# Optimization experiments

Hardware: AMD Instinct MI355X
Metric: run time of the kernel (lower is better)

The kernel has to match this reference:

```python
import jax, jax.numpy as jnp
import numpy as np

B, S, D, H = 4, 2048, 1024, 16
HD = D // H  # head_dim = 64


def setup_inputs() -> dict:
    key = jax.random.key(0)
    ks = jax.random.split(key, 9)
    sc = 1.0 / np.sqrt(D)
    return {
        "x": jax.random.normal(ks[0], (B, S, D), dtype=jnp.float32),
        "Wq": jax.random.normal(ks[1], (D, D), dtype=jnp.float32) * sc,
        "bq": jnp.zeros((D,), dtype=jnp.float32),
        "Wk": jax.random.normal(ks[2], (D, D), dtype=jnp.float32) * sc,
        "bk": jnp.zeros((D,), dtype=jnp.float32),
        "Wv": jax.random.normal(ks[3], (D, D), dtype=jnp.float32) * sc,
        "bv": jnp.zeros((D,), dtype=jnp.float32),
        "Wo": jax.random.normal(ks[4], (D, D), dtype=jnp.float32) * sc,
        "bo": jnp.zeros((D,), dtype=jnp.float32),
    }


def reference(x, Wq, bq, Wk, bk, Wv, bv, Wo, bo):
    # QKV projections (torch Linear: x @ W.T + b), reshape to [B, H, S, HD]
    def proj(W, b):
        return (x @ W.T + b).reshape(B, S, H, HD).transpose(0, 2, 1, 3)

    Q, K, V = proj(Wq, bq), proj(Wk, bk), proj(Wv, bv)
    scores = jnp.einsum("bhqd,bhkd->bhqk", Q, K) / jnp.sqrt(jnp.float32(HD))
    attn = jax.nn.softmax(scores, axis=-1)  # dropout is identity at eval
    ctx = jnp.einsum("bhqk,bhkd->bhqd", attn, V)
    ctx = ctx.transpose(0, 2, 1, 3).reshape(B, S, D)
    out = ctx @ Wo.T + bo
    return out, attn
```

## Files before the change

kernel.cpp:

```cpp
#include <hip/hip_runtime.h>
#include <stdint.h>

#define Mm 8192
#define Dd 1024

typedef unsigned short u16;
typedef __attribute__((ext_vector_type(8))) short bf16x8;
typedef __attribute__((ext_vector_type(4))) float f32x4;
typedef __attribute__((ext_vector_type(4))) u16 u16x4;

__device__ __forceinline__ u16 f2bf(float f) {
  union { float f; uint32_t u; } c; c.f = f;
  uint32_t u = c.u;
  return (u16)((u + 0x7fffu + ((u >> 16) & 1u)) >> 16);
}

__device__ __forceinline__ float EXP2(float x) {
#if __has_builtin(__builtin_amdgcn_exp2f)
  return __builtin_amdgcn_exp2f(x);
#else
  return exp2f(x);
#endif
}

__device__ __forceinline__ float LOG2(float x) {
#if __has_builtin(__builtin_amdgcn_logf)
  return __builtin_amdgcn_logf(x);
#else
  return log2f(x);
#endif
}

__device__ __forceinline__ uint32_t cvtpk(float a, float b) {
  uint32_t r;
  asm("v_cvt_pk_bf16_f32 %0, %1, %2" : "=v"(r) : "v"(a), "v"(b));
  return r;
}

__device__ __forceinline__ void gll16(const void* g, void* l) {
  __builtin_amdgcn_global_load_lds((const __attribute__((address_space(1))) void*)g,
                                   (__attribute__((address_space(3))) void*)l, 16, 0, 0);
}

__global__ void cvt_all(const float* __restrict__ x, const float* __restrict__ wq,
                        const float* __restrict__ wk, const float* __restrict__ wv,
                        const float* __restrict__ wo, u16* __restrict__ out) {
  const int xn4 = 2097152, wn4 = 262144;
  const int total = xn4 + 4 * wn4;
  int i = blockIdx.x * blockDim.x + threadIdx.x;
  int stride = gridDim.x * blockDim.x;
  for (; i < total; i += stride) {
    const float* src; int off;
    if (i < xn4) { src = x; off = i; }
    else {
      int j = i - xn4; int wsel = j >> 18; off = j & (wn4 - 1);
      src = (wsel == 0) ? wq : (wsel == 1) ? wk : (wsel == 2) ? wv : wo;
    }
    float4 v = ((const float4*)src)[off];
    u16x4 o;
    o.x = f2bf(v.x); o.y = f2bf(v.y); o.z = f2bf(v.z); o.w = f2bf(v.w);
    ((u16x4*)out)[i] = o;
  }
}

template<int MODE>
__global__ __launch_bounds__(256) void gemm_bt(
    const u16* __restrict__ A, const u16* __restrict__ Bt,
    const float* __restrict__ bias, void* __restrict__ out,
    int M, int N, int K, float scale)
{
  __shared__ u16 As[128 * 32];
  __shared__ u16 Bs[128 * 32];
  int tiles_n = N >> 7;
  int nwg = (M >> 7) * tiles_n;
  int bid = blockIdx.x;
  { int q = nwg >> 3; bid = (bid & 7) * q + (bid >> 3); }
  int tm = bid / tiles_n, tn = bid % tiles_n;
  int tid = threadIdx.x;
  int wid = tid >> 6, lane = tid & 63;
  int wr = wid >> 1, wc = wid & 1;

  f32x4 acc[4][4] = {};

  int a_row = wr * 64 + (lane & 15);
  int b_row = wc * 64 + (lane & 15);
  int frag_k = (lane >> 4) * 8;

  const u16* ga0 = A + (size_t)(tm * 128 + wid * 32 + (lane >> 2)) * K + (lane & 3) * 8;
  const u16* ga1 = ga0 + (size_t)16 * K;
  const u16* gb0 = Bt + (size_t)(tn * 128 + wid * 32 + (lane >> 2)) * K + (lane & 3) * 8;
  const u16* gb1 = gb0 + (size_t)16 * K;
  u16* lA0 = As + wid * 1024;
  u16* lA1 = As + wid * 1024 + 512;
  u16* lB0 = Bs + wid * 1024;
  u16* lB1 = Bs + wid * 1024 + 512;

  for (int kt = 0; kt < K; kt += 32) {
    gll16(ga0 + kt, lA0);
    gll16(ga1 + kt, lA1);
    gll16(gb0 + kt, lB0);
    gll16(gb1 + kt, lB1);
    __syncthreads();
    bf16x8 af[4], bfr[4];
#pragma unroll
    for (int i = 0; i < 4; i++)
      af[i] = *(const bf16x8*)(As + (a_row + i * 16) * 32 + frag_k);
#pragma unroll
    for (int i = 0; i < 4; i++)
      bfr[i] = *(const bf16x8*)(Bs + (b_row + i * 16) * 32 + frag_k);
#pragma unroll
    for (int i = 0; i < 4; i++)
#pragma unroll
      for (int j = 0; j < 4; j++)
        acc[i][j] = __builtin_amdgcn_mfma_f32_16x16x32_bf16(af[i], bfr[j], acc[i][j], 0, 0, 0);
    __syncthreads();
  }

#pragma unroll
  for (int i = 0; i < 4; i++) {
#pragma unroll
    for (int j = 0; j < 4; j++) {
      int col = tn * 128 + wc * 64 + j * 16 + (lane & 15);
      float bv = bias ? bias[col] : 0.f;
#pragma unroll
      for (int r = 0; r < 4; r++) {
        int row = tm * 128 + wr * 64 + i * 16 + (lane >> 4) * 4 + r;
        float v = (acc[i][j][r] + bv) * scale;
        if (MODE == 0) {
          int b_ = row >> 11, s = row & 2047, h = col >> 6, hd = col & 63;
          ((u16*)out)[(((size_t)(b_ * 16 + h) * 2048 + s) << 6) + hd] = f2bf(v);
        } else if (MODE == 2) {
          int b_ = row >> 11, s = row & 2047, h = col >> 6, hd = col & 63;
          ((u16*)out)[((size_t)(b_ * 16 + h) * 64 + hd) * 2048 + s] = f2bf(v);
        } else {
          ((float*)out)[(size_t)row * N + col] = v;
        }
      }
    }
  }
}

__global__ __launch_bounds__(512) void attn_fused(
    const u16* __restrict__ Qb, const u16* __restrict__ Kb,
    const u16* __restrict__ Vtb, float* __restrict__ attn_out,
    u16* __restrict__ ctxb)
{
  __shared__ u16 Ks[2][4096];
  __shared__ u16 Vs[2][4096];
  __shared__ u16 Ps[8192];

  int bid = blockIdx.x;
  int swz = (bid & 7) * 128 + (bid >> 3);
  int bh = swz >> 4, qt = swz & 15;
  int tid = threadIdx.x, w = tid >> 6, lane = tid & 63;
  int g = lane >> 4, l15 = lane & 15;

  const u16* Qg = Qb + ((size_t)bh * 2048 + qt * 128) * 64;
  const u16* Kg = Kb + (size_t)bh * 2048 * 64;
  const u16* Vg = Vtb + (size_t)bh * 64 * 2048;
  float* Ag = attn_out + ((size_t)bh * 2048 + qt * 128) * 2048;

  int qloc = w * 16 + l15;
  bf16x8 aq0 = *(const bf16x8*)(Qg + (size_t)qloc * 64 + g * 8);
  bf16x8 aq1 = *(const bf16x8*)(Qg + (size_t)qloc * 64 + 32 + g * 8);

  int srow = w * 8 + (lane >> 3);
  int schunk = (lane & 7) ^ (lane >> 3);
  const u16* Ksrc = Kg + (size_t)srow * 64 + schunk * 8;
  const u16* Vsrc = Vg + (size_t)srow * 2048 + schunk * 8;

  float lsum = 0.f;
  gll16(Ksrc, (char*)Ks[0] + w * 1024);
  __syncthreads();
  for (int it = 0; it < 32; ++it) {
    int buf = it & 1;
    if (it < 31) gll16(Ksrc + (size_t)(it + 1) * 4096, (char*)Ks[buf ^ 1] + w * 1024);
    f32x4 s[4] = {};
    const char* Kbase = (const char*)Ks[buf];
#pragma unroll
    for (int t = 0; t < 4; t++) {
      int kr = t * 16 + l15;
      int x = (kr & 7) << 4;
      bf16x8 k0 = *(const bf16x8*)(Kbase + kr * 128 + ((g * 16) ^ x));
      bf16x8 k1 = *(const bf16x8*)(Kbase + kr * 128 + ((64 + g * 16) ^ x));
      s[t] = __builtin_amdgcn_mfma_f32_16x16x32_bf16(k0, aq0, s[t], 0, 0, 0);
      s[t] = __builtin_amdgcn_mfma_f32_16x16x32_bf16(k1, aq1, s[t], 0, 0, 0);
    }
#pragma unroll
    for (int t = 0; t < 4; t++)
#pragma unroll
      for (int r = 0; r < 4; r++) lsum += EXP2(s[t][r]);
    __syncthreads();
  }
  lsum += __shfl_xor(lsum, 16);
  lsum += __shfl_xor(lsum, 32);
  float lr2 = -LOG2(lsum);

  f32x4 ctx[4] = {};
  gll16(Ksrc, (char*)Ks[0] + w * 1024);
  gll16(Vsrc, (char*)Vs[0] + w * 1024);
  __syncthreads();
  int xq = (qloc & 7) << 4;
  char* Pb = (char*)Ps + qloc * 128;
  for (int it = 0; it < 32; ++it) {
    int buf = it & 1;
    if (it < 31) {
      gll16(Ksrc + (size_t)(it + 1) * 4096, (char*)Ks[buf ^ 1] + w * 1024);
      gll16(Vsrc + (size_t)(it + 1) * 64,  (char*)Vs[buf ^ 1] + w * 1024);
    }
    f32x4 s[4] = {};
    const char* Kbase = (const char*)Ks[buf];
#pragma unroll
    for (int t = 0; t < 4; t++) {
      int kr = t * 16 + l15;
      int x = (kr & 7) << 4;
      bf16x8 k0 = *(const bf16x8*)(Kbase + kr * 128 + ((g * 16) ^ x));
      bf16x8 k1 = *(const bf16x8*)(Kbase + kr * 128 + ((64 + g * 16) ^ x));
      s[t] = __builtin_amdgcn_mfma_f32_16x16x32_bf16(k0, aq0, s[t], 0, 0, 0);
      s[t] = __builtin_amdgcn_mfma_f32_16x16x32_bf16(k1, aq1, s[t], 0, 0, 0);
    }
    float* Arow = Ag + (size_t)qloc * 2048 + it * 64 + g * 4;
    uint2 pk[4];
#pragma unroll
    for (int t = 0; t < 4; t++) {
      f32x4 p;
#pragma unroll
      for (int r = 0; r < 4; r++) p[r] = EXP2(s[t][r] + lr2);
      *(f32x4*)(Arow + t * 16) = p;
      pk[t].x = cvtpk(p[0], p[1]);
      pk[t].y = cvtpk(p[2], p[3]);
    }
#pragma unroll
    for (int t = 0; t < 4; t++)
      *(uint2*)(Pb + ((t * 32 + g * 8) ^ xq)) = pk[t];
#pragma unroll
    for (int kk = 0; kk < 2; kk++) {
      bf16x8 ap = *(const bf16x8*)(Pb + ((kk * 64 + g * 16) ^ xq));
#pragma unroll
      for (int t = 0; t < 4; t++) {
        int dr = t * 16 + l15;
        bf16x8 bv = *(const bf16x8*)((const char*)Vs[buf] + dr * 128 + ((kk * 64 + g * 16) ^ ((dr & 7) << 4)));
        ctx[t] = __builtin_amdgcn_mfma_f32_16x16x32_bf16(ap, bv, ctx[t], 0, 0, 0);
      }
    }
    __syncthreads();
  }

  int b_ = bh >> 4, h = bh & 15;
#pragma unroll
  for (int t = 0; t < 4; t++)
#pragma unroll
    for (int r = 0; r < 4; r++) {
      int qg = qt * 128 + w * 16 + g * 4 + r;
      int col = h * 64 + t * 16 + l15;
      ctxb[((size_t)b_ * 2048 + qg) * 1024 + col] = f2bf(ctx[t][r]);
    }
}

extern "C" void kernel_launch(void* const* d_in, const int* in_sizes, int n_in,
                              void* d_out, int out_size, void* d_ws, size_t ws_size,
                              hipStream_t stream) {
  const float* x  = (const float*)d_in[0];
  const float* Wq = (const float*)d_in[1];
  const float* bq = (const float*)d_in[2];
  const float* Wk = (const float*)d_in[3];
  const float* bk = (const float*)d_in[4];
  const float* Wv = (const float*)d_in[5];
  const float* bv = (const float*)d_in[6];
  const float* Wo = (const float*)d_in[7];
  const float* bo = (const float*)d_in[8];

  u16* xb   = (u16*)d_ws;
  u16* Wqb  = xb + (size_t)Mm * Dd;
  u16* Wkb  = Wqb + (size_t)Dd * Dd;
  u16* Wvb  = Wkb + (size_t)Dd * Dd;
  u16* Wob  = Wvb + (size_t)Dd * Dd;
  u16* Qb   = Wob + (size_t)Dd * Dd;
  u16* Kbuf = Qb + (size_t)Mm * Dd;
  u16* Vtb  = Kbuf + (size_t)Mm * Dd;
  u16* ctxb = Vtb + (size_t)Mm * Dd;

  float* out_f = (float*)d_out;
  float* attn_o = out_f + (size_t)Mm * Dd;

  cvt_all<<<2048, 256, 0, stream>>>(x, Wq, Wk, Wv, Wo, xb);

  const float qscale = 0.125f * 1.44269504088896340736f;
  gemm_bt<0><<<512, 256, 0, stream>>>(xb, Wqb, bq, Qb,   Mm, Dd, Dd, qscale);
  gemm_bt<0><<<512, 256, 0, stream>>>(xb, Wkb, bk, Kbuf, Mm, Dd, Dd, 1.0f);
  gemm_bt<2><<<512, 256, 0, stream>>>(xb, Wvb, bv, Vtb,  Mm, Dd, Dd, 1.0f);
  attn_fused<<<1024, 512, 0, stream>>>(Qb, Kbuf, Vtb, attn_o, ctxb);
  gemm_bt<1><<<512, 256, 0, stream>>>(ctxb, Wob, bo, (void*)out_f, Mm, Dd, Dd, 1.0f);
}
```

Baseline: 519.2 us.

## Load K/V fragments directly from global memory, drop LDS staging and barriers

The attention kernel no longer stages K and V tiles through double-buffered shared memory with async loads and __syncthreads. Each wave now reads its MFMA fragments straight from global memory and relies on L1/L2 caching, with a launch-bounds occupancy hint of 4 blocks. The kernel also uses nontemporal stores for the large attention-probability output, and the V-transpose projection epilogue writes four bf16 values as one vector. The aim is to remove LDS traffic and barrier stalls and raise occupancy, at the risk of redundant global/L2 reads by all 8 waves and exposed load latency.

```diff
diff --git a/kernel.cpp b/kernel.cpp
--- a/kernel.cpp
+++ b/kernel.cpp
@@ -122,31 +122,35 @@
     for (int j = 0; j < 4; j++) {
       int col = tn * 128 + wc * 64 + j * 16 + (lane & 15);
       float bv = bias ? bias[col] : 0.f;
-#pragma unroll
-      for (int r = 0; r < 4; r++) {
-        int row = tm * 128 + wr * 64 + i * 16 + (lane >> 4) * 4 + r;
-        float v = (acc[i][j][r] + bv) * scale;
-        if (MODE == 0) {
-          int b_ = row >> 11, s = row & 2047, h = col >> 6, hd = col & 63;
-          ((u16*)out)[(((size_t)(b_ * 16 + h) * 2048 + s) << 6) + hd] = f2bf(v);
-        } else if (MODE == 2) {
-          int b_ = row >> 11, s = row & 2047, h = col >> 6, hd = col & 63;
-          ((u16*)out)[((size_t)(b_ * 16 + h) * 64 + hd) * 2048 + s] = f2bf(v);
-        } else {
-          ((float*)out)[(size_t)row * N + col] = v;
+      if (MODE == 2) {
+        int row0 = tm * 128 + wr * 64 + i * 16 + (lane >> 4) * 4;
+        int b_ = row0 >> 11, s0 = row0 & 2047, h = col >> 6, hd = col & 63;
+        u16x4 o;
+#pragma unroll
+        for (int r = 0; r < 4; r++) o[r] = f2bf((acc[i][j][r] + bv) * scale);
+        *(u16x4*)&((u16*)out)[((size_t)(b_ * 16 + h) * 64 + hd) * 2048 + s0] = o;
+      } else {
+#pragma unroll
+        for (int r = 0; r < 4; r++) {
+          int row = tm * 128 + wr * 64 + i * 16 + (lane >> 4) * 4 + r;
+          float v = (acc[i][j][r] + bv) * scale;
+          if (MODE == 0) {
+            int b_ = row >> 11, s = row & 2047, h = col >> 6, hd = col & 63;
+            ((u16*)out)[(((size_t)(b_ * 16 + h) * 2048 + s) << 6) + hd] = f2bf(v);
+          } else {
+            ((float*)out)[(size_t)row * N + col] = v;
+          }
         }
       }
     }
   }
 }
 
-__global__ __launch_bounds__(512) void attn_fused(
+__global__ __launch_bounds__(512, 4) void attn_fused(
     const u16* __restrict__ Qb, const u16* __restrict__ Kb,
     const u16* __restrict__ Vtb, float* __restrict__ attn_out,
     u16* __restrict__ ctxb)
 {
-  __shared__ u16 Ks[2][4096];
-  __shared__ u16 Vs[2][4096];
   __shared__ u16 Ps[8192];
 
   int bid = blockIdx.x;
@@ -164,25 +168,17 @@
   bf16x8 aq0 = *(const bf16x8*)(Qg + (size_t)qloc * 64 + g * 8);
   bf16x8 aq1 = *(const bf16x8*)(Qg + (size_t)qloc * 64 + 32 + g * 8);
 
-  int srow = w * 8 + (lane >> 3);
-  int schunk = (lane & 7) ^ (lane >> 3);
-  const u16* Ksrc = Kg + (size_t)srow * 64 + schunk * 8;
-  const u16* Vsrc = Vg + (size_t)srow * 2048 + schunk * 8;
+  const u16* Kf = Kg + (size_t)l15 * 64 + g * 8;
+  const u16* Vf = Vg + (size_t)l15 * 2048 + g * 8;
 
   float lsum = 0.f;
-  gll16(Ksrc, (char*)Ks[0] + w * 1024);
-  __syncthreads();
   for (int it = 0; it < 32; ++it) {
-    int buf = it & 1;
-    if (it < 31) gll16(Ksrc + (size_t)(it + 1) * 4096, (char*)Ks[buf ^ 1] + w * 1024);
+    const u16* kp = Kf + (size_t)it * 4096;
     f32x4 s[4] = {};
-    const char* Kbase = (const char*)Ks[buf];
 #pragma unroll
     for (int t = 0; t < 4; t++) {
-      int kr = t * 16 + l15;
-      int x = (kr & 7) << 4;
-      bf16x8 k0 = *(const bf16x8*)(Kbase + kr * 128 + ((g * 16) ^ x));
-      bf16x8 k1 = *(const bf16x8*)(Kbase + kr * 128 + ((64 + g * 16) ^ x));
+      bf16x8 k0 = *(const bf16x8*)(kp + t * 1024);
+      bf16x8 k1 = *(const bf16x8*)(kp + t * 1024 + 32);
       s[t] = __builtin_amdgcn_mfma_f32_16x16x32_bf16(k0, aq0, s[t], 0, 0, 0);
       s[t] = __builtin_amdgcn_mfma_f32_16x16x32_bf16(k1, aq1, s[t], 0, 0, 0);
     }
@@ -190,60 +186,46 @@
     for (int t = 0; t < 4; t++)
 #pragma unroll
       for (int r = 0; r < 4; r++) lsum += EXP2(s[t][r]);
-    __syncthreads();
   }
   lsum += __shfl_xor(lsum, 16);
   lsum += __shfl_xor(lsum, 32);
   float lr2 = -LOG2(lsum);
 
   f32x4 ctx[4] = {};
-  gll16(Ksrc, (char*)Ks[0] + w * 1024);
-  gll16(Vsrc, (char*)Vs[0] + w * 1024);
-  __syncthreads();
   int xq = (qloc & 7) << 4;
   char* Pb = (char*)Ps + qloc * 128;
   for (int it = 0; it < 32; ++it) {
-    int buf = it & 1;
-    if (it < 31) {
-      gll16(Ksrc + (size_t)(it + 1) * 4096, (char*)Ks[buf ^ 1] + w * 1024);
-      gll16(Vsrc + (size_t)(it + 1) * 64,  (char*)Vs[buf ^ 1] + w * 1024);
-    }
+    const u16* kp = Kf + (size_t)it * 4096;
     f32x4 s[4] = {};
-    const char* Kbase = (const char*)Ks[buf];
 #pragma unroll
     for (int t = 0; t < 4; t++) {
-      int kr = t * 16 + l15;
-      int x = (kr & 7) << 4;
-      bf16x8 k0 = *(const bf16x8*)(Kbase + kr * 128 + ((g * 16) ^ x));
-      bf16x8 k1 = *(const bf16x8*)(Kbase + kr * 128 + ((64 + g * 16) ^ x));
+      bf16x8 k0 = *(const bf16x8*)(kp + t * 1024);
+      bf16x8 k1 = *(const bf16x8*)(kp + t * 1024 + 32);
       s[t] = __builtin_amdgcn_mfma_f32_16x16x32_bf16(k0, aq0, s[t], 0, 0, 0);
       s[t] = __builtin_amdgcn_mfma_f32_16x16x32_bf16(k1, aq1, s[t], 0, 0, 0);
     }
     float* Arow = Ag + (size_t)qloc * 2048 + it * 64 + g * 4;
-    uint2 pk[4];
 #pragma unroll
     for (int t = 0; t < 4; t++) {
       f32x4 p;
 #pragma unroll
       for (int r = 0; r < 4; r++) p[r] = EXP2(s[t][r] + lr2);
-      *(f32x4*)(Arow + t * 16) = p;
-      pk[t].x = cvtpk(p[0], p[1]);
-      pk[t].y = cvtpk(p[2], p[3]);
-    }
-#pragma unroll
-    for (int t = 0; t < 4; t++)
-      *(uint2*)(Pb + ((t * 32 + g * 8) ^ xq)) = pk[t];
+      __builtin_nontemporal_store(p, (f32x4*)(Arow + t * 16));
+      uint2 pk;
+      pk.x = cvtpk(p[0], p[1]);
+      pk.y = cvtpk(p[2], p[3]);
+      *(uint2*)(Pb + ((t * 32 + g * 8) ^ xq)) = pk;
+    }
+    const u16* vp = Vf + (size_t)it * 64;
 #pragma unroll
     for (int kk = 0; kk < 2; kk++) {
       bf16x8 ap = *(const bf16x8*)(Pb + ((kk * 64 + g * 16) ^ xq));
 #pragma unroll
       for (int t = 0; t < 4; t++) {
-        int dr = t * 16 + l15;
-        bf16x8 bv = *(const bf16x8*)((const char*)Vs[buf] + dr * 128 + ((kk * 64 + g * 16) ^ ((dr & 7) << 4)));
+        bf16x8 bv = *(const bf16x8*)(vp + t * 32768 + kk * 32);
         ctx[t] = __builtin_amdgcn_mfma_f32_16x16x32_bf16(ap, bv, ctx[t], 0, 0, 0);
       }
     }
-    __syncthreads();
   }
 
   int b_ = bh >> 4, h = bh & 15;
```

Result: slower. 838.9 us (+61.6%).

## Refine attention pipeline waits, add priority hints, nontemporal attn stores, vector V^T stores

Applied to the files above, without the earlier changes.

Replaces __syncthreads with explicit vmcnt waits plus raw barriers, so the prefetch of the next K/V tile stays in flight while the current tile is consumed. It also adds s_setprio around the MFMA sections, splits the exp-sum into four accumulators, and writes the large fp32 attention matrix with nontemporal stores. Separately, the transposed-V projection epilogue packs four bf16 values into one vector store. The unconditional wraparound prefetch on the last iteration adds redundant loads, and the hand-tuned vmcnt counts risk races if the compiler emits a different number of memory ops.

```diff
diff --git a/kernel.cpp b/kernel.cpp
--- a/kernel.cpp
+++ b/kernel.cpp
@@ -122,18 +122,24 @@
     for (int j = 0; j < 4; j++) {
       int col = tn * 128 + wc * 64 + j * 16 + (lane & 15);
       float bv = bias ? bias[col] : 0.f;
-#pragma unroll
-      for (int r = 0; r < 4; r++) {
-        int row = tm * 128 + wr * 64 + i * 16 + (lane >> 4) * 4 + r;
-        float v = (acc[i][j][r] + bv) * scale;
-        if (MODE == 0) {
-          int b_ = row >> 11, s = row & 2047, h = col >> 6, hd = col & 63;
-          ((u16*)out)[(((size_t)(b_ * 16 + h) * 2048 + s) << 6) + hd] = f2bf(v);
-        } else if (MODE == 2) {
-          int b_ = row >> 11, s = row & 2047, h = col >> 6, hd = col & 63;
-          ((u16*)out)[((size_t)(b_ * 16 + h) * 64 + hd) * 2048 + s] = f2bf(v);
-        } else {
-          ((float*)out)[(size_t)row * N + col] = v;
+      if (MODE == 2) {
+        int row0 = tm * 128 + wr * 64 + i * 16 + (lane >> 4) * 4;
+        int b_ = row0 >> 11, s0 = row0 & 2047, h = col >> 6, hd = col & 63;
+        u16x4 o;
+#pragma unroll
+        for (int r = 0; r < 4; r++) o[r] = f2bf((acc[i][j][r] + bv) * scale);
+        *(u16x4*)&((u16*)out)[((size_t)(b_ * 16 + h) * 64 + hd) * 2048 + s0] = o;
+      } else {
+#pragma unroll
+        for (int r = 0; r < 4; r++) {
+          int row = tm * 128 + wr * 64 + i * 16 + (lane >> 4) * 4 + r;
+          float v = (acc[i][j][r] + bv) * scale;
+          if (MODE == 0) {
+            int b_ = row >> 11, s = row & 2047, h = col >> 6, hd = col & 63;
+            ((u16*)out)[(((size_t)(b_ * 16 + h) * 2048 + s) << 6) + hd] = f2bf(v);
+          } else {
+            ((float*)out)[(size_t)row * N + col] = v;
+          }
         }
       }
     }
@@ -169,14 +175,19 @@
   const u16* Ksrc = Kg + (size_t)srow * 64 + schunk * 8;
   const u16* Vsrc = Vg + (size_t)srow * 2048 + schunk * 8;
 
-  float lsum = 0.f;
+  float ls0 = 0.f, ls1 = 0.f, ls2 = 0.f, ls3 = 0.f;
   gll16(Ksrc, (char*)Ks[0] + w * 1024);
-  __syncthreads();
+  asm volatile("s_waitcnt vmcnt(0)" ::: "memory");
+  __builtin_amdgcn_s_barrier();
   for (int it = 0; it < 32; ++it) {
     int buf = it & 1;
-    if (it < 31) gll16(Ksrc + (size_t)(it + 1) * 4096, (char*)Ks[buf ^ 1] + w * 1024);
+    int nx = (it + 1) & 31;
+    gll16(Ksrc + (size_t)nx * 4096, (char*)Ks[buf ^ 1] + w * 1024);
+    asm volatile("s_waitcnt vmcnt(1)" ::: "memory");
+    __builtin_amdgcn_s_barrier();
     f32x4 s[4] = {};
     const char* Kbase = (const char*)Ks[buf];
+    __builtin_amdgcn_s_setprio(1);
 #pragma unroll
     for (int t = 0; t < 4; t++) {
       int kr = t * 16 + l15;
@@ -186,30 +197,37 @@
       s[t] = __builtin_amdgcn_mfma_f32_16x16x32_bf16(k0, aq0, s[t], 0, 0, 0);
       s[t] = __builtin_amdgcn_mfma_f32_16x16x32_bf16(k1, aq1, s[t], 0, 0, 0);
     }
-#pragma unroll
-    for (int t = 0; t < 4; t++)
-#pragma unroll
-      for (int r = 0; r < 4; r++) lsum += EXP2(s[t][r]);
-    __syncthreads();
-  }
+    __builtin_amdgcn_s_setprio(0);
+#pragma unroll
+    for (int r = 0; r < 4; r++) {
+      ls0 += EXP2(s[0][r]); ls1 += EXP2(s[1][r]);
+      ls2 += EXP2(s[2][r]); ls3 += EXP2(s[3][r]);
+    }
+    asm volatile("" ::: "memory");
+    __builtin_amdgcn_s_barrier();
+  }
+  float lsum = (ls0 + ls1) + (ls2 + ls3);
   lsum += __shfl_xor(lsum, 16);
   lsum += __shfl_xor(lsum, 32);
   float lr2 = -LOG2(lsum);
 
   f32x4 ctx[4] = {};
+  int xq = (qloc & 7) << 4;
+  char* Pb = (char*)Ps + qloc * 128;
   gll16(Ksrc, (char*)Ks[0] + w * 1024);
   gll16(Vsrc, (char*)Vs[0] + w * 1024);
-  __syncthreads();
-  int xq = (qloc & 7) << 4;
-  char* Pb = (char*)Ps + qloc * 128;
+  asm volatile("s_waitcnt vmcnt(0)" ::: "memory");
+  __builtin_amdgcn_s_barrier();
   for (int it = 0; it < 32; ++it) {
     int buf = it & 1;
-    if (it < 31) {
-      gll16(Ksrc + (size_t)(it + 1) * 4096, (char*)Ks[buf ^ 1] + w * 1024);
-      gll16(Vsrc + (size_t)(it + 1) * 64,  (char*)Vs[buf ^ 1] + w * 1024);
-    }
+    int nx = (it + 1) & 31;
+    gll16(Ksrc + (size_t)nx * 4096, (char*)Ks[buf ^ 1] + w * 1024);
+    gll16(Vsrc + (size_t)nx * 64,  (char*)Vs[buf ^ 1] + w * 1024);
+    asm volatile("s_waitcnt vmcnt(6)" ::: "memory");
+    __builtin_amdgcn_s_barrier();
     f32x4 s[4] = {};
     const char* Kbase = (const char*)Ks[buf];
+    __builtin_amdgcn_s_setprio(1);
 #pragma unroll
     for (int t = 0; t < 4; t++) {
       int kr = t * 16 + l15;
@@ -219,20 +237,20 @@
       s[t] = __builtin_amdgcn_mfma_f32_16x16x32_bf16(k0, aq0, s[t], 0, 0, 0);
       s[t] = __builtin_amdgcn_mfma_f32_16x16x32_bf16(k1, aq1, s[t], 0, 0, 0);
     }
+    __builtin_amdgcn_s_setprio(0);
     float* Arow = Ag + (size_t)qloc * 2048 + it * 64 + g * 4;
-    uint2 pk[4];
 #pragma unroll
     for (int t = 0; t < 4; t++) {
       f32x4 p;
 #pragma unroll
       for (int r = 0; r < 4; r++) p[r] = EXP2(s[t][r] + lr2);
-      *(f32x4*)(Arow + t * 16) = p;
-      pk[t].x = cvtpk(p[0], p[1]);
-      pk[t].y = cvtpk(p[2], p[3]);
-    }
-#pragma unroll
-    for (int t = 0; t < 4; t++)
-      *(uint2*)(Pb + ((t * 32 + g * 8) ^ xq)) = pk[t];
+      __builtin_nontemporal_store(p, (f32x4*)(Arow + t * 16));
+      uint2 pk;
+      pk.x = cvtpk(p[0], p[1]);
+      pk.y = cvtpk(p[2], p[3]);
+      *(uint2*)(Pb + ((t * 32 + g * 8) ^ xq)) = pk;
+    }
+    __builtin_amdgcn_s_setprio(1);
 #pragma unroll
     for (int kk = 0; kk < 2; kk++) {
       bf16x8 ap = *(const bf16x8*)(Pb + ((kk * 64 + g * 16) ^ xq));
@@ -243,7 +261,9 @@
         ctx[t] = __builtin_amdgcn_mfma_f32_16x16x32_bf16(ap, bv, ctx[t], 0, 0, 0);
       }
     }
-    __syncthreads();
+    __builtin_amdgcn_s_setprio(0);
+    asm volatile("" ::: "memory");
+    __builtin_amdgcn_s_barrier();
   }
 
   int b_ = bh >> 4, h = bh & 15;
```

Result: faster. 470.9 us (-9.3%).
